# Kernel tuning notes

Hardware: AMD Instinct MI355X
Metric: run time of the kernel (lower is better)

Reference implementation:

```python
import jax, jax.numpy as jnp
import numpy as np

SCALING = 1.0


def setup_inputs() -> dict:
    key = jax.random.key(0)
    k1, k2, k3, k4, k5, k6 = jax.random.split(key, 6)
    in_f, out_f, r = 4096, 4096, 32
    nnz = r * (in_f + out_f)  # 262144
    x = jax.random.normal(k1, (4, 2048, in_f), dtype=jnp.float32)
    weight = jax.random.normal(k2, (out_f, in_f), dtype=jnp.float32) * 0.02
    bias = jax.random.normal(k3, (out_f,), dtype=jnp.float32) * 0.02
    shira_weight = jax.random.normal(k4, (nnz,), dtype=jnp.float32) * 0.02
    rows = jax.random.randint(k5, (1, nnz), 0, out_f, dtype=jnp.int32)
    cols = jax.random.randint(k6, (1, nnz), 0, in_f, dtype=jnp.int32)
    shira_indices = jnp.concatenate([rows, cols], axis=0)  # [2, nnz]
    return {"x": x, "weight": weight, "bias": bias,
            "shira_weight": shira_weight, "shira_indices": shira_indices}


def reference(x, weight, bias, shira_weight, shira_indices):
    # delta = sparse_coo(indices, shira_weight * scaling) densified into weight copy
    new_weight = weight.at[shira_indices[0], shira_indices[1]].add(shira_weight * SCALING)
    # F.linear: x @ W^T + b
    return jnp.einsum('bsi,oi->bso', x, new_weight) + bias
```

## Files before the change

kernel.cpp:

```cpp
#include <hip/hip_runtime.h>
#include <hip/hip_bf16.h>
#include <stdint.h>

typedef float v4f __attribute__((ext_vector_type(4)));
typedef short v8s __attribute__((ext_vector_type(8)));

#define GEMM_M 8192
#define GEMM_N 4096
#define GEMM_K 4096
#define BM 256
#define BN 256
#define BK 64
#define NT (GEMM_K / BK)


__device__ __forceinline__ uint16_t f2bf(float f) {
    union { float f; uint32_t u; } v; v.f = f;
    uint32_t r = v.u + 0x7FFFu + ((v.u >> 16) & 1u);
    return (uint16_t)(r >> 16);
}

__device__ __forceinline__ float bf2f(uint16_t h) {
    union { uint32_t u; float f; } v; v.u = ((uint32_t)h) << 16;
    return v.f;
}

__device__ __forceinline__ void cvt8(const float* __restrict__ s, uint16_t* __restrict__ d) {
    float4 a = ((const float4*)s)[0];
    float4 b = ((const float4*)s)[1];
    union { v8s v; uint16_t u[8]; } o;
    o.u[0] = f2bf(a.x); o.u[1] = f2bf(a.y); o.u[2] = f2bf(a.z); o.u[3] = f2bf(a.w);
    o.u[4] = f2bf(b.x); o.u[5] = f2bf(b.y); o.u[6] = f2bf(b.z); o.u[7] = f2bf(b.w);
    *(v8s*)d = o.v;
}

__global__ void prep_cvt_kernel(const float* __restrict__ X, const float* __restrict__ W,
                                uint16_t* __restrict__ Xb, uint16_t* __restrict__ Wb,
                                size_t x8) {
    size_t i = (size_t)blockIdx.x * blockDim.x + threadIdx.x;
    if (i < x8) {
        cvt8(X + i * 8, Xb + i * 8);
    } else {
        size_t j = i - x8;
        cvt8(W + j * 8, Wb + j * 8);
    }
}

__global__ void scatter_bf16_kernel(uint16_t* __restrict__ Wb, const float* __restrict__ vals,
                                    const int* __restrict__ rows, const int* __restrict__ cols,
                                    int nnz) {
    int i = blockIdx.x * blockDim.x + threadIdx.x;
    if (i >= nnz) return;
    size_t idx = (size_t)rows[i] * GEMM_K + cols[i];
    uint32_t* addr = (uint32_t*)Wb + (idx >> 1);
    const bool hi = idx & 1;
    const float v = vals[i];
    uint32_t cur = *addr, assumed;
    do {
        assumed = cur;
        uint16_t h = hi ? (uint16_t)(assumed >> 16) : (uint16_t)(assumed & 0xFFFFu);
        uint16_t nh = f2bf(bf2f(h) + v);
        uint32_t nw = hi ? ((assumed & 0x0000FFFFu) | ((uint32_t)nh << 16))
                         : ((assumed & 0xFFFF0000u) | (uint32_t)nh);
        if (nw == assumed) break;
        cur = atomicCAS(addr, assumed, nw);
    } while (cur != assumed);
}


__device__ __forceinline__ void gload_lds16(const void* g, void* lds) {
    __builtin_amdgcn_global_load_lds(
        (const __attribute__((address_space(1))) void*)(uintptr_t)g,
        (__attribute__((address_space(3))) void*)(uintptr_t)lds,
        16, 0, 0);
}

__global__ __launch_bounds__(512, 2) void gemm_bt_kernel(
    const uint16_t* __restrict__ A,
    const uint16_t* __restrict__ B,
    const float* __restrict__ bias,
    float* __restrict__ C)
{
    __shared__ __attribute__((aligned(16))) uint16_t As[2][2][128 * BK];
    __shared__ __attribute__((aligned(16))) uint16_t Bs[2][2][128 * BK];

    const int tid  = threadIdx.x;
    const int lane = tid & 63;
    const int wid  = tid >> 6;
    const int wm2  = wid >> 1;
    const int wn2  = wid & 1;
    const int lrow = lane & 15;
    const int quad = lane >> 4;
    const int xr   = lane & 7;

    const int bid = blockIdx.x;
    const int swz = (bid & 7) * 64 + (bid >> 3);
    const int m0  = (swz >> 4) * BM;
    const int n0  = (swz & 15) * BN;

    const int srow = wid * 16 + (lane >> 3);
    const int skc  = ((lane & 7) ^ (lane >> 3)) * 8;
    const uint16_t* gA = A + (size_t)(m0 + srow) * GEMM_K + skc;
    const uint16_t* gB = B + (size_t)(n0 + srow) * GEMM_K + skc;
    const int ldso = wid * 1024 + lane * 8;

#define STAGE(gbase, hrow, s, ldshalf)  do {                                   \
        const uint16_t* _g = (gbase) + (size_t)(hrow) * GEMM_K + (s) * BK;     \
        uint16_t* _l = (ldshalf) + ldso;                                       \
        gload_lds16(_g, _l);                                                   \
        gload_lds16(_g + (size_t)8 * GEMM_K, _l + 512);                        \
    } while (0)

    v4f acc00[2][4], acc10[2][4], acc01[2][4], acc11[2][4];
#pragma unroll
    for (int mi = 0; mi < 2; ++mi)
#pragma unroll
        for (int nj = 0; nj < 4; ++nj) {
            acc00[mi][nj] = (v4f){0.f, 0.f, 0.f, 0.f};
            acc10[mi][nj] = (v4f){0.f, 0.f, 0.f, 0.f};
            acc01[mi][nj] = (v4f){0.f, 0.f, 0.f, 0.f};
            acc11[mi][nj] = (v4f){0.f, 0.f, 0.f, 0.f};
        }

    v8s a0F[2][2], a1F[2][2], bF[4][2];

#define LDA(dst, hp) do {                                                      \
        _Pragma("unroll")                                                      \
        for (int mi = 0; mi < 2; ++mi)                                         \
        _Pragma("unroll")                                                      \
        for (int ks = 0; ks < 2; ++ks) {                                       \
            const int rh = wm2 * 32 + mi * 16 + lrow;                          \
            const int c  = ks * 4 + quad;                                      \
            dst[mi][ks] = *(const v8s*)((hp) + rh * BK + ((c ^ xr) << 3));     \
        } } while (0)

#define LDB(hp) do {                                                           \
        _Pragma("unroll")                                                      \
        for (int nj = 0; nj < 4; ++nj)                                         \
        _Pragma("unroll")                                                      \
        for (int ks = 0; ks < 2; ++ks) {                                       \
            const int rh = wn2 * 64 + nj * 16 + lrow;                          \
            const int c  = ks * 4 + quad;                                      \
            bF[nj][ks] = *(const v8s*)((hp) + rh * BK + ((c ^ xr) << 3));      \
        } } while (0)

#define MM(accq, aT) do {                                                      \
        _Pragma("unroll")                                                      \
        for (int ks = 0; ks < 2; ++ks)                                         \
        _Pragma("unroll")                                                      \
        for (int mi = 0; mi < 2; ++mi)                                         \
        _Pragma("unroll")                                                      \
        for (int nj = 0; nj < 4; ++nj)                                         \
            accq[mi][nj] = __builtin_amdgcn_mfma_f32_16x16x32_bf16(            \
                aT[mi][ks], bF[nj][ks], accq[mi][nj], 0, 0, 0);                \
    } while (0)

#define BAR()   __builtin_amdgcn_s_barrier()
#define LGKM0() asm volatile("s_waitcnt lgkmcnt(0)" ::: "memory")
#define VM6()   asm volatile("s_waitcnt vmcnt(6)" ::: "memory")
#define SCHED() __builtin_amdgcn_sched_barrier(0)
#define PRIO(p) __builtin_amdgcn_s_setprio(p)

    STAGE(gA, 0,   0, &As[0][0][0]);
    STAGE(gA, 128, 0, &As[0][1][0]);
    STAGE(gB, 0,   0, &Bs[0][0][0]);
    STAGE(gB, 128, 0, &Bs[0][1][0]);
    SCHED();
    STAGE(gA, 0,   1, &As[1][0][0]);
    STAGE(gA, 128, 1, &As[1][1][0]);
    STAGE(gB, 0,   1, &Bs[1][0][0]);
    VM6();
    BAR();

#define TILE(t, b) do {                                                        \
        const int s1 = ((t) + 1) & (NT - 1);                                   \
        const int s2 = ((t) + 2) & (NT - 1);                                   \
                                         \
        LDA(a0F, &As[b][0][0]);                                                \
        LDB(&Bs[b][0][0]);                                                     \
        STAGE(gB, 128, s1, &Bs[(b) ^ 1][1][0]);                                \
        BAR();                                                                 \
        PRIO(1); MM(acc00, a0F); PRIO(0);                                      \
        LGKM0();                                                               \
        BAR();                                                                 \
                                          \
        LDA(a1F, &As[b][1][0]);                                                \
        STAGE(gA, 0, s2, &As[b][0][0]);                                        \
        BAR();                                                                 \
        PRIO(1); MM(acc10, a1F); PRIO(0);                                      \
        LGKM0();                                                               \
        BAR();                                                                 \
                                          \
        LDB(&Bs[b][1][0]);                                                     \
        STAGE(gA, 128, s2, &As[b][1][0]);                                      \
        BAR();                                                                 \
        PRIO(1); MM(acc01, a0F); PRIO(0);                                      \
        LGKM0();                                                               \
        BAR();                                                                 \
                \
        STAGE(gB, 0, s2, &Bs[b][0][0]);                                        \
        VM6();                                                                 \
        BAR();                                                                 \
        PRIO(1); MM(acc11, a1F); PRIO(0);                                      \
    } while (0)

    for (int t = 0; t < NT; t += 2) {
        TILE(t, 0);
        TILE(t + 1, 1);
    }

#define WR(accq, QM, QN) do {                                                  \
        _Pragma("unroll")                                                      \
        for (int nj = 0; nj < 4; ++nj) {                                       \
            const int col = n0 + (QN) * 128 + wn2 * 64 + nj * 16 + lrow;       \
            const float bj = bias[col];                                        \
            _Pragma("unroll")                                                  \
            for (int mi = 0; mi < 2; ++mi) {                                   \
                const int row = m0 + (QM) * 128 + wm2 * 32 + mi * 16 + quad * 4; \
                float* cp = C + (size_t)row * GEMM_N + col;                    \
                _Pragma("unroll")                                              \
                for (int r = 0; r < 4; ++r)                                    \
                    cp[(size_t)r * GEMM_N] = accq[mi][nj][r] + bj;             \
            }                                                                  \
        } } while (0)

    WR(acc00, 0, 0);
    WR(acc10, 1, 0);
    WR(acc01, 0, 1);
    WR(acc11, 1, 1);

#undef STAGE
#undef LDA
#undef LDB
#undef MM
#undef BAR
#undef LGKM0
#undef VM6
#undef SCHED
#undef PRIO
#undef TILE
#undef WR
}


extern "C" void kernel_launch(void* const* d_in, const int* in_sizes, int n_in,
                              void* d_out, int out_size, void* d_ws, size_t ws_size,
                              hipStream_t stream) {
    const float* x      = (const float*)d_in[0];
    const float* weight = (const float*)d_in[1];
    const float* bias   = (const float*)d_in[2];
    const float* sw     = (const float*)d_in[3];
    const int*   sidx   = (const int*)d_in[4];
    const int nnz = in_sizes[3];

    const size_t welems = (size_t)GEMM_N * GEMM_K;
    const size_t xelems = (size_t)GEMM_M * GEMM_K;

    uint16_t* Wb = (uint16_t*)d_ws;
    uint16_t* Xb = (uint16_t*)((char*)d_ws + welems * sizeof(uint16_t));

    const size_t x8 = xelems / 8;
    const size_t w8 = welems / 8;
    const int prep_blocks = (int)((x8 + w8) / 256);

    prep_cvt_kernel<<<dim3(prep_blocks), 256, 0, stream>>>(x, weight, Xb, Wb, x8);
    scatter_bf16_kernel<<<dim3((nnz + 255) / 256), 256, 0, stream>>>(
        Wb, sw, sidx, sidx + nnz, nnz);
    gemm_bt_kernel<<<dim3((GEMM_M / BM) * (GEMM_N / BN)), 512, 0, stream>>>(
        Xb, Wb, bias, (float*)d_out);
}
```

Baseline: 499.2 us.

## Double-buffer B fragments and prefetch next tile's LDS reads across MFMA phases

Splits the B register fragment into two buffers so LDS reads for the next quadrant can be issued before the current MFMA block runs. It also moves the first A/B fragment loads of each tile to the end of the previous tile. The explicit lgkmcnt(0) waits and several barriers are removed, relying on compiler-inserted waits. This aims to hide LDS latency behind MFMA work and cut synchronisation, at the cost of more VGPRs. With fewer barriers there is a risk of LDS read/write hazards between the staged global-to-LDS loads and the fragment reads.

```diff
diff --git a/kernel.cpp b/kernel.cpp
--- a/kernel.cpp
+++ b/kernel.cpp
@@ -122,7 +122,7 @@
             acc11[mi][nj] = (v4f){0.f, 0.f, 0.f, 0.f};
         }
 
-    v8s a0F[2][2], a1F[2][2], bF[4][2];
+    v8s a0F[2][2], a1F[2][2], bF0[4][2], bF1[4][2];
 
 #define LDA(dst, hp) do {                                                      \
         _Pragma("unroll")                                                      \
@@ -134,17 +134,17 @@
             dst[mi][ks] = *(const v8s*)((hp) + rh * BK + ((c ^ xr) << 3));     \
         } } while (0)
 
-#define LDB(hp) do {                                                           \
+#define LDB(dst, hp) do {                                                      \
         _Pragma("unroll")                                                      \
         for (int nj = 0; nj < 4; ++nj)                                         \
         _Pragma("unroll")                                                      \
         for (int ks = 0; ks < 2; ++ks) {                                       \
             const int rh = wn2 * 64 + nj * 16 + lrow;                          \
             const int c  = ks * 4 + quad;                                      \
-            bF[nj][ks] = *(const v8s*)((hp) + rh * BK + ((c ^ xr) << 3));      \
+            dst[nj][ks] = *(const v8s*)((hp) + rh * BK + ((c ^ xr) << 3));     \
         } } while (0)
 
-#define MM(accq, aT) do {                                                      \
+#define MM(accq, aT, bT) do {                                                  \
         _Pragma("unroll")                                                      \
         for (int ks = 0; ks < 2; ++ks)                                         \
         _Pragma("unroll")                                                      \
@@ -152,11 +152,10 @@
         _Pragma("unroll")                                                      \
         for (int nj = 0; nj < 4; ++nj)                                         \
             accq[mi][nj] = __builtin_amdgcn_mfma_f32_16x16x32_bf16(            \
-                aT[mi][ks], bF[nj][ks], accq[mi][nj], 0, 0, 0);                \
+                aT[mi][ks], bT[nj][ks], accq[mi][nj], 0, 0, 0);                \
     } while (0)
 
 #define BAR()   __builtin_amdgcn_s_barrier()
-#define LGKM0() asm volatile("s_waitcnt lgkmcnt(0)" ::: "memory")
 #define VM6()   asm volatile("s_waitcnt vmcnt(6)" ::: "memory")
 #define SCHED() __builtin_amdgcn_sched_barrier(0)
 #define PRIO(p) __builtin_amdgcn_s_setprio(p)
@@ -171,37 +170,33 @@
     STAGE(gB, 0,   1, &Bs[1][0][0]);
     VM6();
     BAR();
+    LDA(a0F, &As[0][0][0]);
+    LDB(bF0, &Bs[0][0][0]);
 
 #define TILE(t, b) do {                                                        \
         const int s1 = ((t) + 1) & (NT - 1);                                   \
         const int s2 = ((t) + 2) & (NT - 1);                                   \
-                                         \
-        LDA(a0F, &As[b][0][0]);                                                \
-        LDB(&Bs[b][0][0]);                                                     \
+                       \
+        LDA(a1F, &As[b][1][0]);                                                \
+        BAR();                                                                 \
         STAGE(gB, 128, s1, &Bs[(b) ^ 1][1][0]);                                \
-        BAR();                                                                 \
-        PRIO(1); MM(acc00, a0F); PRIO(0);                                      \
-        LGKM0();                                                               \
-        BAR();                                                                 \
-                                          \
-        LDA(a1F, &As[b][1][0]);                                                \
+        PRIO(1); MM(acc00, a0F, bF0); PRIO(0);                                 \
+                                 \
+        LDB(bF1, &Bs[b][1][0]);                                                \
+        BAR();                                                                 \
         STAGE(gA, 0, s2, &As[b][0][0]);                                        \
-        BAR();                                                                 \
-        PRIO(1); MM(acc10, a1F); PRIO(0);                                      \
-        LGKM0();                                                               \
-        BAR();                                                                 \
-                                          \
-        LDB(&Bs[b][1][0]);                                                     \
+        PRIO(1); MM(acc10, a1F, bF0); PRIO(0);                                 \
+                                       \
+        BAR();                                                                 \
         STAGE(gA, 128, s2, &As[b][1][0]);                                      \
-        BAR();                                                                 \
-        PRIO(1); MM(acc01, a0F); PRIO(0);                                      \
-        LGKM0();                                                               \
-        BAR();                                                                 \
-                \
+        PRIO(1); MM(acc01, a0F, bF1); PRIO(0);                                 \
+         \
         STAGE(gB, 0, s2, &Bs[b][0][0]);                                        \
         VM6();                                                                 \
         BAR();                                                                 \
-        PRIO(1); MM(acc11, a1F); PRIO(0);                                      \
+        LDA(a0F, &As[(b) ^ 1][0][0]);                                          \
+        LDB(bF0, &Bs[(b) ^ 1][0][0]);                                          \
+        PRIO(1); MM(acc11, a1F, bF1); PRIO(0);                                 \
     } while (0)
 
     for (int t = 0; t < NT; t += 2) {
@@ -234,7 +229,6 @@
 #undef LDB
 #undef MM
 #undef BAR
-#undef LGKM0
 #undef VM6
 #undef SCHED
 #undef PRIO
```

New measurement: 496.2 us. Within noise of the previous version (-0.6%).
